# Kernel optimization log

Hardware: AMD Instinct MI355X
Metric: run time of the kernel (lower is better)

The kernel has to match this reference:

```python
import jax, jax.numpy as jnp
import numpy as np

N = 100000   # nodes
E = 1000000  # edges
IN, H, OUT = 256, 64, 16


def setup_inputs() -> dict:
    key = jax.random.key(0)
    k0, k1, k2, k3 = jax.random.split(key, 4)
    x = jax.random.normal(k0, (N, IN), jnp.float32)
    edge_index = jax.random.randint(k1, (2, E), 0, N)
    # GCNConv parameters (glorot-ish weights, zero bias as in PyG defaults)
    W1 = jax.random.normal(k2, (IN, H), jnp.float32) / np.sqrt(IN).astype(np.float32)
    b1 = jnp.zeros((H,), jnp.float32)
    W2 = jax.random.normal(k3, (H, OUT), jnp.float32) / np.sqrt(H).astype(np.float32)
    b2 = jnp.zeros((OUT,), jnp.float32)
    return {"x": x, "edge_index": edge_index, "W1": W1, "b1": b1, "W2": W2, "b2": b2}


def gcn_conv(x, W, b, src, dst, n):
    # PyG GCNConv: h = x @ W; out[v] = sum_{(u->v)} norm(u,v) * h[u] + b
    h = x @ W                                    # [n, out]
    deg = jnp.zeros((n,), h.dtype).at[dst].add(1.0)
    dinv = jnp.where(deg > 0, jax.lax.rsqrt(deg), 0.0)
    norm = dinv[src] * dinv[dst]                 # [E+n] symmetric normalization
    msg = h[src] * norm[:, None]                 # gather + scale
    agg = jax.ops.segment_sum(msg, dst, num_segments=n)  # scatter-add
    return agg + b


def reference(x, edge_index, W1, b1, W2, b2):
    n = x.shape[0]
    # add self-loops (PyG GCNConv default add_self_loops=True)
    loops = jnp.arange(n, dtype=edge_index.dtype)
    src = jnp.concatenate([edge_index[0], loops])
    dst = jnp.concatenate([edge_index[1], loops])
    h = gcn_conv(x, W1, b1, src, dst, n)
    h = jax.nn.relu(h)  # F.dropout is identity in eval mode (training=False)
    return gcn_conv(h, W2, b2, src, dst, n)
```

## Files before the change

### kernel.cpp

```cpp
#include <hip/hip_runtime.h>

namespace {
constexpr int NN  = 100000;
constexpr int NE  = 1000000;
constexpr int INF = 256;
constexpr int HF  = 64;
constexpr int OF  = 16;
constexpr int SCAN_CHUNK = 1024;
constexpr int NBLK = (NN + SCAN_CHUNK - 1) / SCAN_CHUNK;
constexpr int NSEG = 8;
constexpr int SEGW = (NN + NSEG - 1) / NSEG;
constexpr int CNTW = 100096;
constexpr int ZBLK = (CNTW / 4 + 255) / 256;
}

typedef __attribute__((ext_vector_type(8))) short     sh8;
typedef __attribute__((ext_vector_type(4))) float     f32x4;
typedef __attribute__((ext_vector_type(8))) unsigned short us8;

__device__ __forceinline__ unsigned short f2bf(float f) {
    unsigned int u = __builtin_bit_cast(unsigned int, f);
    u += 0x7FFFu + ((u >> 16) & 1u);
    return (unsigned short)(u >> 16);
}
__device__ __forceinline__ float bf2f(unsigned short s) {
    return __builtin_bit_cast(float, (unsigned int)s << 16);
}

__global__ void k_pre(int* __restrict__ cnt, const float* __restrict__ W1,
                      unsigned short* __restrict__ wt_g) {
    int b = blockIdx.x, t = threadIdx.x;
    if (b < ZBLK) {
        int i = (b * 256 + t) * 4;
        if (i < CNTW) *(int4*)(cnt + i) = (int4){0, 0, 0, 0};
    } else {
        int idx = (b - ZBLK) * 256 + t;
        int c = idx >> 8, k = idx & 255;
        wt_g[idx] = f2bf(W1[(size_t)k * HF + c]);
    }
}

__global__ void k_hist(const int* __restrict__ dst, int* __restrict__ cnt) {
    int b     = blockIdx.x;
    int seg   = b & (NSEG - 1);
    int chunk = b >> 3;
    int e = chunk * 256 + threadIdx.x;
    if (e < NE) {
        int d = dst[e];
        if ((unsigned)d / (unsigned)SEGW == (unsigned)seg)
            atomicAdd(&cnt[d], 1);
    }
}

__global__ __launch_bounds__(256) void k_reduce(const int* __restrict__ cnt,
                                                int* __restrict__ bsum,
                                                float* __restrict__ dinv) {
    int t = threadIdx.x;
    int i0 = blockIdx.x * SCAN_CHUNK + t * 4;
    int s = 0;
    float dv[4] = {0.f, 0.f, 0.f, 0.f};
    #pragma unroll
    for (int q = 0; q < 4; ++q) {
        if (i0 + q < NN) {
            int c = cnt[i0 + q];
            s += c;
            dv[q] = rsqrtf((float)(c + 1));
        }
    }
    if (i0 + 3 < NN) *(float4*)(dinv + i0) = (float4){dv[0], dv[1], dv[2], dv[3]};
    else { for (int q = 0; q < 4; ++q) if (i0 + q < NN) dinv[i0 + q] = dv[q]; }
    #pragma unroll
    for (int off = 32; off > 0; off >>= 1) s += __shfl_down(s, off);
    __shared__ int wsum[4];
    int lane = t & 63, wid = t >> 6;
    if (lane == 0) wsum[wid] = s;
    __syncthreads();
    if (t == 0) bsum[blockIdx.x] = wsum[0] + wsum[1] + wsum[2] + wsum[3];
}

__global__ void k_partials(int* __restrict__ bsum) {
    int l = threadIdx.x;
    int a0 = (l < NBLK) ? bsum[l] : 0;
    int b0 = (64 + l < NBLK) ? bsum[64 + l] : 0;
    int a = a0, b = b0;
    #pragma unroll
    for (int off = 1; off < 64; off <<= 1) {
        int na = __shfl_up(a, off); if (l >= off) a += na;
        int nb = __shfl_up(b, off); if (l >= off) b += nb;
    }
    int tot = __shfl(a, 63);
    if (l < NBLK) bsum[l] = a - a0;
    if (64 + l < NBLK) bsum[64 + l] = tot + b - b0;
}

__global__ __launch_bounds__(256) void k_scan(const int* __restrict__ cnt,
                                              const int* __restrict__ bsum,
                                              int* __restrict__ rowptr,
                                              int* __restrict__ cursor) {
    int t = threadIdx.x;
    int i0 = blockIdx.x * SCAN_CHUNK + t * 4;
    int v0 = 0, v1 = 0, v2 = 0, v3 = 0;
    if (i0 + 0 < NN) v0 = cnt[i0 + 0];
    if (i0 + 1 < NN) v1 = cnt[i0 + 1];
    if (i0 + 2 < NN) v2 = cnt[i0 + 2];
    if (i0 + 3 < NN) v3 = cnt[i0 + 3];
    int tsum = v0 + v1 + v2 + v3;
    int lane = t & 63, wid = t >> 6;
    int incl = tsum;
    #pragma unroll
    for (int off = 1; off < 64; off <<= 1) {
        int n = __shfl_up(incl, off);
        if (lane >= off) incl += n;
    }
    __shared__ int wsum[4];
    if (lane == 63) wsum[wid] = incl;
    __syncthreads();
    int woff = 0;
    for (int w = 0; w < wid; ++w) woff += wsum[w];
    int excl = woff + (incl - tsum) + bsum[blockIdx.x];
    int e0 = excl, e1 = e0 + v0, e2 = e1 + v1, e3 = e2 + v2;
    if (i0 + 0 < NN) { rowptr[i0 + 0] = e0; cursor[i0 + 0] = e0; }
    if (i0 + 1 < NN) { rowptr[i0 + 1] = e1; cursor[i0 + 1] = e1; }
    if (i0 + 2 < NN) { rowptr[i0 + 2] = e2; cursor[i0 + 2] = e2; }
    if (i0 + 3 < NN) { rowptr[i0 + 3] = e3; cursor[i0 + 3] = e3; }
    if (i0 + 3 == NN - 1) rowptr[NN] = e3 + v3;
}

__global__ __launch_bounds__(256) void k_scatter(const int* __restrict__ src,
                                                 const int* __restrict__ dst,
                                                 int* __restrict__ cursor,
                                                 int* __restrict__ eidx) {
    int b     = blockIdx.x;
    int seg   = b & (NSEG - 1);
    int chunk = b >> 3;
    int e = chunk * 256 + threadIdx.x;
    if (e < NE) {
        int d = dst[e];
        if ((unsigned)d / (unsigned)SEGW == (unsigned)seg) {
            int p = atomicAdd(&cursor[d], 1);
            eidx[p] = src[e];
        }
    }
}

__global__ __launch_bounds__(256, 4) void k_gemm1(const float* __restrict__ x,
                                                  const unsigned short* __restrict__ wt_g,
                                                  unsigned short* __restrict__ h1) {
    __shared__ unsigned short wt[64 * 264];
    int t = threadIdx.x;
    int w = t >> 6, l = t & 63;
    int row0 = blockIdx.x * 128;

    #pragma unroll
    for (int p = 0; p < 8; ++p) {
        int T   = p * 256 + t;
        int c   = T >> 5;
        int kb8 = T & 31;
        *(us8*)(wt + c * 264 + kb8 * 8) = *(const us8*)(wt_g + c * 256 + kb8 * 8);
    }
    __syncthreads();

    int m = l & 15;
    int g = l >> 4;
    int gr0 = row0 + w * 32 + m;      if (gr0 > NN - 1) gr0 = NN - 1;
    int gr1 = row0 + w * 32 + 16 + m; if (gr1 > NN - 1) gr1 = NN - 1;
    const float* p0 = x + (size_t)gr0 * INF + g * 8;
    const float* p1 = x + (size_t)gr1 * INF + g * 8;

    f32x4 acc[2][4];
    #pragma unroll
    for (int i = 0; i < 2; ++i)
        #pragma unroll
        for (int j = 0; j < 4; ++j) acc[i][j] = (f32x4){0.f, 0.f, 0.f, 0.f};

    #pragma unroll 2
    for (int kb = 0; kb < INF; kb += 32) {
        float4 u0 = *(const float4*)(p0 + kb);
        float4 u1 = *(const float4*)(p0 + kb + 4);
        float4 u2 = *(const float4*)(p1 + kb);
        float4 u3 = *(const float4*)(p1 + kb + 4);
        us8 a0u = { f2bf(u0.x), f2bf(u0.y), f2bf(u0.z), f2bf(u0.w),
                    f2bf(u1.x), f2bf(u1.y), f2bf(u1.z), f2bf(u1.w) };
        us8 a1u = { f2bf(u2.x), f2bf(u2.y), f2bf(u2.z), f2bf(u2.w),
                    f2bf(u3.x), f2bf(u3.y), f2bf(u3.z), f2bf(u3.w) };
        sh8 a0 = __builtin_bit_cast(sh8, a0u);
        sh8 a1 = __builtin_bit_cast(sh8, a1u);
        #pragma unroll
        for (int nt = 0; nt < 4; ++nt) {
            sh8 b = *(const sh8*)(wt + (nt * 16 + m) * 264 + kb + g * 8);
            acc[0][nt] = __builtin_amdgcn_mfma_f32_16x16x32_bf16(a0, b, acc[0][nt], 0, 0, 0);
            acc[1][nt] = __builtin_amdgcn_mfma_f32_16x16x32_bf16(a1, b, acc[1][nt], 0, 0, 0);
        }
    }

    #pragma unroll
    for (int mt = 0; mt < 2; ++mt) {
        #pragma unroll
        for (int r = 0; r < 4; ++r) {
            int gr = row0 + w * 32 + mt * 16 + (l >> 4) * 4 + r;
            if (gr < NN) {
                #pragma unroll
                for (int nt = 0; nt < 4; ++nt)
                    h1[(size_t)gr * HF + nt * 16 + (l & 15)] = f2bf(acc[mt][nt][r]);
            }
        }
    }
}

__global__ __launch_bounds__(256) void k_gather1(const int* __restrict__ rowptr,
                                                 const int* __restrict__ eidx,
                                                 const float* __restrict__ dinv,
                                                 const unsigned short* __restrict__ h1,
                                                 const float* __restrict__ b1,
                                                 const float* __restrict__ W2,
                                                 float* __restrict__ h2) {
    __shared__ float w2L[HF * OF];
    __shared__ float hrL[4][HF];
    int t = threadIdx.x;
    *(float4*)(w2L + t * 4) = *(const float4*)(W2 + t * 4);

    int wid  = t >> 6;
    int v    = blockIdx.x * 4 + wid;
    int lane = t & 63;
    int eslot = lane >> 3;
    int fg    = lane & 7;
    int beg = rowptr[v], end = rowptr[v + 1];
    float acc[8] = {};
    for (int i = beg + eslot; i < end; i += 8) {
        int s = eidx[i];
        float wgt = dinv[s];
        us8 hv = *(const us8*)(h1 + (size_t)s * HF + fg * 8);
        #pragma unroll
        for (int q = 0; q < 8; ++q) acc[q] += wgt * bf2f(hv[q]);
    }
    #pragma unroll
    for (int mk = 8; mk <= 32; mk <<= 1)
        #pragma unroll
        for (int q = 0; q < 8; ++q) acc[q] += __shfl_xor(acc[q], mk);

    if (lane < 8) {
        float dv = dinv[v], sl = dv * dv;
        us8 hv = *(const us8*)(h1 + (size_t)v * HF + fg * 8);
        #pragma unroll
        for (int q = 0; q < 8; ++q) {
            float val = dv * acc[q] + sl * bf2f(hv[q]) + b1[fg * 8 + q];
            hrL[wid][fg * 8 + q] = val > 0.f ? val : 0.f;
        }
    }
    __syncthreads();

    int j  = lane & 15;
    int kh = lane >> 4;
    const float* hr = hrL[wid];
    float p = 0.f;
    #pragma unroll
    for (int kk = 0; kk < 16; ++kk)
        p += hr[kh * 16 + kk] * w2L[(kh * 16 + kk) * OF + j];
    p += __shfl_xor(p, 16);
    p += __shfl_xor(p, 32);
    if (lane < 16) h2[(size_t)v * OF + j] = p;
}

__global__ __launch_bounds__(256) void k_gather2(const int* __restrict__ rowptr,
                                                 const int* __restrict__ eidx,
                                                 const float* __restrict__ dinv,
                                                 const float* __restrict__ h2,
                                                 const float* __restrict__ b2,
                                                 float* __restrict__ out) {
    int gid   = blockIdx.x * 256 + threadIdx.x;
    int v     = gid >> 6;
    int lane  = threadIdx.x & 63;
    int eslot = lane >> 2;
    int fg    = lane & 3;
    int beg = rowptr[v], end = rowptr[v + 1];
    float4 acc = {0.f, 0.f, 0.f, 0.f};
    for (int i = beg + eslot; i < end; i += 16) {
        int s = eidx[i];
        float w = dinv[s];
        float4 hv = *(const float4*)(h2 + (size_t)s * OF + fg * 4);
        acc.x += w * hv.x; acc.y += w * hv.y; acc.z += w * hv.z; acc.w += w * hv.w;
    }
    #pragma unroll
    for (int m = 4; m <= 32; m <<= 1) {
        acc.x += __shfl_xor(acc.x, m);
        acc.y += __shfl_xor(acc.y, m);
        acc.z += __shfl_xor(acc.z, m);
        acc.w += __shfl_xor(acc.w, m);
    }
    if (eslot == 0) {
        float dv = dinv[v];
        float sl = dv * dv;
        float4 hv = *(const float4*)(h2 + (size_t)v * OF + fg * 4);
        float4 bv = *(const float4*)(b2 + fg * 4);
        float4 o;
        o.x = dv * acc.x + sl * hv.x + bv.x;
        o.y = dv * acc.y + sl * hv.y + bv.y;
        o.z = dv * acc.z + sl * hv.z + bv.z;
        o.w = dv * acc.w + sl * hv.w + bv.w;
        *(float4*)(out + (size_t)v * OF + fg * 4) = o;
    }
}

extern "C" void kernel_launch(void* const* d_in, const int* in_sizes, int n_in,
                              void* d_out, int out_size, void* d_ws, size_t ws_size,
                              hipStream_t stream) {
    const float* x   = (const float*)d_in[0];
    const int*   ei  = (const int*)d_in[1];
    const int*   src = ei;
    const int*   dst = ei + NE;
    const float* W1  = (const float*)d_in[2];
    const float* b1  = (const float*)d_in[3];
    const float* W2  = (const float*)d_in[4];
    const float* b2  = (const float*)d_in[5];
    float* out = (float*)d_out;

    float* dinv  = (float*)d_ws;
    unsigned short* h1b = (unsigned short*)(dinv + CNTW);
    float* h2    = (float*)(h1b + (size_t)NN * HF);
    int*   cnt   = (int*)(h2 + (size_t)NN * OF);
    int*   rowptr = cnt + CNTW;
    int*   cursor = rowptr + 100352;
    int*   eidx  = cursor + CNTW;
    int*   bsum  = eidx + NE;
    unsigned short* wt_g = (unsigned short*)(bsum + 128);

    k_pre<<<ZBLK + 64, 256, 0, stream>>>(cnt, W1, wt_g);
    k_hist<<<((NE + 255) / 256) * NSEG, 256, 0, stream>>>(dst, cnt);
    k_reduce<<<NBLK, 256, 0, stream>>>(cnt, bsum, dinv);
    k_partials<<<1, 64, 0, stream>>>(bsum);
    k_scan<<<NBLK, 256, 0, stream>>>(cnt, bsum, rowptr, cursor);
    k_scatter<<<((NE + 255) / 256) * NSEG, 256, 0, stream>>>(src, dst, cursor, eidx);

    k_gemm1<<<(NN + 127) / 128, 256, 0, stream>>>(x, wt_g, h1b);
    k_gather1<<<NN / 4, 256, 0, stream>>>(rowptr, eidx, dinv, h1b, b1, W2, h2);

    k_gather2<<<(NN * HF) / 256, 256, 0, stream>>>(rowptr, eidx, dinv, h2, b2, out);
}
```

Measured before the change: 206.1 us.

## Assign 8 threads per node in gather1, processing 32 nodes per block

Layer-1 aggregation now gives each node an 8-lane group that walks its edges serially, replacing the full 64-lane wavefront per node that split edges across 8 slots. This drops the cross-lane shuffle reduction and the lanes left idle on low-degree nodes, since average degree is about 10. The second-layer projection becomes a per-thread 64-length dot product over a padded shared tile. The cost is a longer serial edge loop per thread, with less memory-level parallelism per node and divergence on high-degree nodes.

```diff
diff --git a/kernel.cpp b/kernel.cpp
--- a/kernel.cpp
+++ b/kernel.cpp
@@ -215,50 +215,44 @@
                                                  const float* __restrict__ W2,
                                                  float* __restrict__ h2) {
     __shared__ float w2L[HF * OF];
-    __shared__ float hrL[4][HF];
+    __shared__ float hrL[32][HF + 4];
     int t = threadIdx.x;
     *(float4*)(w2L + t * 4) = *(const float4*)(W2 + t * 4);
 
-    int wid  = t >> 6;
-    int v    = blockIdx.x * 4 + wid;
-    int lane = t & 63;
-    int eslot = lane >> 3;
-    int fg    = lane & 7;
+    int nodeL = t >> 3;
+    int fg    = t & 7;
+    int v     = blockIdx.x * 32 + nodeL;
     int beg = rowptr[v], end = rowptr[v + 1];
+
     float acc[8] = {};
-    for (int i = beg + eslot; i < end; i += 8) {
+    for (int i = beg; i < end; ++i) {
         int s = eidx[i];
         float wgt = dinv[s];
         us8 hv = *(const us8*)(h1 + (size_t)s * HF + fg * 8);
         #pragma unroll
         for (int q = 0; q < 8; ++q) acc[q] += wgt * bf2f(hv[q]);
     }
-    #pragma unroll
-    for (int mk = 8; mk <= 32; mk <<= 1)
-        #pragma unroll
-        for (int q = 0; q < 8; ++q) acc[q] += __shfl_xor(acc[q], mk);
-
-    if (lane < 8) {
+
+    {
         float dv = dinv[v], sl = dv * dv;
         us8 hv = *(const us8*)(h1 + (size_t)v * HF + fg * 8);
         #pragma unroll
         for (int q = 0; q < 8; ++q) {
             float val = dv * acc[q] + sl * bf2f(hv[q]) + b1[fg * 8 + q];
-            hrL[wid][fg * 8 + q] = val > 0.f ? val : 0.f;
+            hrL[nodeL][fg * 8 + q] = val > 0.f ? val : 0.f;
         }
     }
     __syncthreads();
 
-    int j  = lane & 15;
-    int kh = lane >> 4;
-    const float* hr = hrL[wid];
-    float p = 0.f;
-    #pragma unroll
-    for (int kk = 0; kk < 16; ++kk)
-        p += hr[kh * 16 + kk] * w2L[(kh * 16 + kk) * OF + j];
-    p += __shfl_xor(p, 16);
-    p += __shfl_xor(p, 32);
-    if (lane < 16) h2[(size_t)v * OF + j] = p;
+    #pragma unroll
+    for (int T = t; T < 512; T += 256) {
+        int n = T >> 4, j = T & 15;
+        const float* hr = hrL[n];
+        float p = 0.f;
+        #pragma unroll
+        for (int k = 0; k < HF; ++k) p += hr[k] * w2L[k * OF + j];
+        h2[(size_t)(blockIdx.x * 32 + n) * OF + j] = p;
+    }
 }
 
 __global__ __launch_bounds__(256) void k_gather2(const int* __restrict__ rowptr,
@@ -332,7 +326,7 @@
     k_scatter<<<((NE + 255) / 256) * NSEG, 256, 0, stream>>>(src, dst, cursor, eidx);
 
     k_gemm1<<<(NN + 127) / 128, 256, 0, stream>>>(x, wt_g, h1b);
-    k_gather1<<<NN / 4, 256, 0, stream>>>(rowptr, eidx, dinv, h1b, b1, W2, h2);
+    k_gather1<<<NN / 32, 256, 0, stream>>>(rowptr, eidx, dinv, h1b, b1, W2, h2);
 
     k_gather2<<<(NN * HF) / 256, 256, 0, stream>>>(rowptr, eidx, dinv, h2, b2, out);
 }
```

New measurement: 188.5 us. -8.6%, faster.
